# Kernel tuning notes

Measured on AMD Instinct MI355X. Metric: run time of the kernel, lower is better.

## Reference

```python
import jax, jax.numpy as jnp
import numpy as np

N_NODES = 50000
N_EDGES = 800000
IN_FT = 256
OUT_FT = 128


def setup_inputs() -> dict:
    key = jax.random.key(0)
    k_seq, k_src, k_dst, k_val, k_w = jax.random.split(key, 5)
    seq = jax.random.normal(k_seq, (N_NODES, IN_FT), dtype=jnp.float32)
    edge_src = jax.random.randint(k_src, (N_EDGES,), 0, N_NODES, dtype=jnp.int64)
    edge_dst = jax.random.randint(k_dst, (N_EDGES,), 0, N_NODES, dtype=jnp.int64)
    edge_val = jax.random.uniform(k_val, (N_EDGES,), dtype=jnp.float32)
    # xavier_uniform for Linear(in_ft, out_ft): limit = sqrt(6/(in+out))
    limit = float(np.sqrt(6.0 / (IN_FT + OUT_FT)))
    W = jax.random.uniform(k_w, (OUT_FT, IN_FT), minval=-limit, maxval=limit, dtype=jnp.float32)
    bias = jnp.zeros((OUT_FT,), dtype=jnp.float32)
    prelu_a = jnp.full((1,), 0.25, dtype=jnp.float32)  # nn.PReLU default slope
    return {"seq": seq, "edge_src": edge_src, "edge_dst": edge_dst,
            "edge_val": edge_val, "W": W, "bias": bias, "prelu_a": prelu_a}


def reference(seq, edge_src, edge_dst, edge_val, W, bias, prelu_a):
    # seq_fts = fc(seq): [N, out_ft]
    seq_fts = jnp.einsum('ni,oi->no', seq, W)
    # sparse spmm: out[dst] += val * seq_fts[src]
    msgs = seq_fts[edge_src] * edge_val[:, None]          # [E, out_ft]
    out = jax.ops.segment_sum(msgs, edge_dst, num_segments=seq.shape[0])
    out = out + bias                                       # bias add
    # PReLU with learnable slope a
    return jnp.where(out >= 0, out, prelu_a * out)
```

## Files before the change

### kernel.cpp

```cpp
#include <hip/hip_runtime.h>
#include <hip/hip_bf16.h>

#define N_NODES 50000
#define N_EDGES 800000
#define IN_FT 256
#define OUT_FT 128

typedef __bf16 bf16;
typedef __attribute__((ext_vector_type(8))) __bf16 bf16x8;
typedef __attribute__((ext_vector_type(4))) float floatx4;

static __device__ inline unsigned short f2bf_bits(float f) {
    unsigned u = __float_as_uint(f);
    return (unsigned short)((u + 0x7FFFu + ((u >> 16) & 1u)) >> 16);
}

#define P 256
#define CHUNK (N_EDGES / P)
#define NBUCK ((N_NODES + 255) / 256)
#define NSCAN (NBUCK * P)
#define GM 128
#define GEMM_BLKS ((N_NODES + GM - 1) / GM)
#define WP 264

__global__ __launch_bounds__(256) void k_prep(const float* __restrict__ W,
                                              const int* __restrict__ dst,
                                              unsigned short* __restrict__ Wb,
                                              int* __restrict__ cnt,
                                              unsigned long long* __restrict__ status,
                                              int* __restrict__ ticket) {
    const int b = blockIdx.x, t = threadIdx.x;
    if (b < P) {
        __shared__ int h[NBUCK];
        if (t < NBUCK) h[t] = 0;
        __syncthreads();
        const int base = b * CHUNK;
        for (int i = t; i < CHUNK; i += 256)
            atomicAdd(&h[dst[base + i] >> 8], 1);
        __syncthreads();
        if (t < NBUCK) cnt[t * P + b] = h[t];
    } else if (b == P) {
        if (t < NBUCK) status[t] = 0ull;
        if (t == 255) *ticket = 0;
    } else {
        int i = (b - P - 1) * 256 + t;
        float4 v = ((const float4*)W)[i];
        ushort4 o;
        o.x = f2bf_bits(v.x); o.y = f2bf_bits(v.y);
        o.z = f2bf_bits(v.z); o.w = f2bf_bits(v.w);
        ((ushort4*)Wb)[i] = o;
    }
}

__global__ __launch_bounds__(512) void k_gemm_scan(const float* __restrict__ seq,
                                                   const unsigned short* __restrict__ Wb,
                                                   unsigned short* __restrict__ seq_fts,
                                                   const int* __restrict__ cnt,
                                                   int* __restrict__ cnt_off,
                                                   int* __restrict__ partoff,
                                                   unsigned long long* __restrict__ status,
                                                   int* __restrict__ ticket) {
    const int t = threadIdx.x;
    if (blockIdx.x < GEMM_BLKS) {
        __shared__ bf16 Wlds[128 * WP];
        {
            const int row = t >> 2, c0 = (t & 3) * 64;
            const unsigned short* src = Wb + row * IN_FT + c0;
            bf16* dstp = Wlds + row * WP + c0;
#pragma unroll
            for (int c = 0; c < 8; ++c)
                *(uint4*)(dstp + c * 8) = *(const uint4*)(src + c * 8);
        }
        const int lane = t & 63;
        const int wave = t >> 6;
        const int quad = lane >> 4;
        const int l16  = lane & 15;

        int arow = blockIdx.x * GM + wave * 16 + l16;
        if (arow >= N_NODES) arow = 0;
        const float* ap = seq + (size_t)arow * IN_FT + quad * 8;
        bf16x8 afr[8];
#pragma unroll
        for (int s = 0; s < 8; ++s) {
            float4 v0 = *(const float4*)(ap + s * 32);
            float4 v1 = *(const float4*)(ap + s * 32 + 4);
            bf16x8 a;
            a[0] = (bf16)v0.x; a[1] = (bf16)v0.y; a[2] = (bf16)v0.z; a[3] = (bf16)v0.w;
            a[4] = (bf16)v1.x; a[5] = (bf16)v1.y; a[6] = (bf16)v1.z; a[7] = (bf16)v1.w;
            afr[s] = a;
        }
        __syncthreads();

        const int mbase = blockIdx.x * GM + wave * 16;
#pragma unroll
        for (int tt = 0; tt < 8; ++tt) {
            floatx4 acc = {0.f, 0.f, 0.f, 0.f};
            const bf16* bp = Wlds + (tt * 16 + l16) * WP + quad * 8;
#pragma unroll
            for (int s = 0; s < 8; ++s) {
                bf16x8 bfr = *(const bf16x8*)(bp + s * 32);
                acc = __builtin_amdgcn_mfma_f32_16x16x32_bf16(afr[s], bfr, acc, 0, 0, 0);
            }
#pragma unroll
            for (int r = 0; r < 4; ++r) {
                int m = mbase + quad * 4 + r;
                if (m < N_NODES)
                    seq_fts[(size_t)m * OUT_FT + tt * 16 + l16] = f2bf_bits(acc[r]);
            }
        }
    } else {
        __shared__ int lds2[256];
        __shared__ int stile;
        __shared__ unsigned run_sh;
        if (t == 0) stile = atomicAdd(ticket, 1);
        __syncthreads();
        const int j = stile;
        int v = (t < 256) ? cnt[j * 256 + t] : 0;
        if (t < 256) lds2[t] = v;
        __syncthreads();
        for (int s = 1; s < 256; s <<= 1) {
            int add = (t < 256 && t >= s) ? lds2[t - s] : 0;
            __syncthreads();
            if (t < 256) lds2[t] += add;
            __syncthreads();
        }
        const unsigned total = (unsigned)lds2[255];
        if (t == 0) {
            if (j == 0) {
                atomicExch(&status[0], ((unsigned long long)total << 2) | 2ull);
                run_sh = 0;
            } else {
                atomicExch(&status[j], ((unsigned long long)total << 2) | 1ull);
                unsigned running = 0;
                int k = j - 1;
                for (;;) {
                    unsigned long long s = atomicAdd(&status[k], 0ull);
                    unsigned st = (unsigned)(s & 3ull);
                    if (st == 0u) { __builtin_amdgcn_s_sleep(1); continue; }
                    running += (unsigned)(s >> 2);
                    if (st == 2u) break;
                    --k;
                }
                atomicExch(&status[j],
                           ((unsigned long long)(running + total) << 2) | 2ull);
                run_sh = running;
            }
        }
        __syncthreads();
        const int base = (int)run_sh;
        if (t < 256) cnt_off[j * 256 + t] = base + lds2[t] - v;
        if (t == 0) partoff[j] = base;
        if (t == 0 && j == NBUCK - 1) partoff[NBUCK] = base + (int)total;
    }
}

__global__ __launch_bounds__(256) void k_pscat(const int* __restrict__ src,
                                               const int* __restrict__ dst,
                                               const float* __restrict__ val,
                                               const int* __restrict__ cnt_off,
                                               uint2* __restrict__ part_ev) {
    __shared__ int off[NBUCK];
    const int t = threadIdx.x;
    if (t < NBUCK) off[t] = cnt_off[t * P + blockIdx.x];
    __syncthreads();
    const int base = blockIdx.x * CHUNK;
    for (int i = t; i < CHUNK; i += 256) {
        int e = base + i;
        int d = dst[e];
        int pos = atomicAdd(&off[d >> 8], 1);
        unsigned x = (unsigned)(unsigned short)src[e]
                   | ((unsigned)f2bf_bits(val[e]) << 16);
        part_ev[pos] = make_uint2(x, (unsigned)d);
    }
}

__global__ __launch_bounds__(256) void k_fill2(const uint2* __restrict__ part_ev,
                                               const int* __restrict__ partoff,
                                               int* __restrict__ row_ptr,
                                               unsigned* __restrict__ csr_ev) {
    __shared__ int cnt[256];
    __shared__ int lds[256];
    __shared__ int cur[256];
    const int b = blockIdx.x, t = threadIdx.x;
    const int start = partoff[b];
    const int end   = partoff[b + 1];
    cnt[t] = 0;
    __syncthreads();
    for (int i = start + t; i < end; i += 256)
        atomicAdd(&cnt[part_ev[i].y & 255u], 1);
    __syncthreads();
    int v = cnt[t];
    lds[t] = v;
    __syncthreads();
#pragma unroll
    for (int s = 1; s < 256; s <<= 1) {
        int t2 = (t >= s) ? lds[t - s] : 0;
        __syncthreads();
        lds[t] += t2;
        __syncthreads();
    }
    int base = start + lds[t] - v;
    int n = b * 256 + t;
    if (n <= N_NODES) row_ptr[n] = base;
    cur[t] = base;
    __syncthreads();
    for (int i = start + t; i < end; i += 256) {
        uint2 r = part_ev[i];
        int pos = atomicAdd(&cur[r.y & 255u], 1);
        csr_ev[pos] = r.x;
    }
}

#define GW 4
__global__ __launch_bounds__(64 * GW) void k_gather(const unsigned* __restrict__ fts,
                                                    const int* __restrict__ row_ptr,
                                                    const unsigned* __restrict__ csr_ev,
                                                    const float* __restrict__ bias,
                                                    const float* __restrict__ prelu_a,
                                                    float* __restrict__ out) {
    const int wave = threadIdx.x >> 6;
    const int lane = threadIdx.x & 63;
    const int n = blockIdx.x * GW + wave;
    if (n >= N_NODES) return;
    const int s0 = row_ptr[n];
    const int s1 = row_ptr[n + 1];
    float acc0 = 0.f, acc1 = 0.f;
    int j = s0;
    for (; j + 3 < s1; j += 4) {
        unsigned w0 = csr_ev[j],     w1 = csr_ev[j + 1];
        unsigned w2 = csr_ev[j + 2], w3 = csr_ev[j + 3];
        unsigned p0 = fts[(w0 & 0xFFFFu) * 64u + lane];
        unsigned p1 = fts[(w1 & 0xFFFFu) * 64u + lane];
        unsigned p2 = fts[(w2 & 0xFFFFu) * 64u + lane];
        unsigned p3 = fts[(w3 & 0xFFFFu) * 64u + lane];
        float v0 = __uint_as_float(w0 & 0xFFFF0000u);
        float v1 = __uint_as_float(w1 & 0xFFFF0000u);
        float v2 = __uint_as_float(w2 & 0xFFFF0000u);
        float v3 = __uint_as_float(w3 & 0xFFFF0000u);
        acc0 += v0 * __uint_as_float(p0 << 16);
        acc1 += v0 * __uint_as_float(p0 & 0xFFFF0000u);
        acc0 += v1 * __uint_as_float(p1 << 16);
        acc1 += v1 * __uint_as_float(p1 & 0xFFFF0000u);
        acc0 += v2 * __uint_as_float(p2 << 16);
        acc1 += v2 * __uint_as_float(p2 & 0xFFFF0000u);
        acc0 += v3 * __uint_as_float(p3 << 16);
        acc1 += v3 * __uint_as_float(p3 & 0xFFFF0000u);
    }
    for (; j < s1; ++j) {
        unsigned w0 = csr_ev[j];
        unsigned p0 = fts[(w0 & 0xFFFFu) * 64u + lane];
        float v0 = __uint_as_float(w0 & 0xFFFF0000u);
        acc0 += v0 * __uint_as_float(p0 << 16);
        acc1 += v0 * __uint_as_float(p0 & 0xFFFF0000u);
    }
    float2 b = *(const float2*)&bias[lane * 2];
    float a = prelu_a[0];
    float x0 = acc0 + b.x;
    float x1 = acc1 + b.y;
    x0 = (x0 >= 0.f) ? x0 : a * x0;
    x1 = (x1 >= 0.f) ? x1 : a * x1;
    *(float2*)&out[(size_t)n * OUT_FT + lane * 2] = make_float2(x0, x1);
}

extern "C" void kernel_launch(void* const* d_in, const int* in_sizes, int n_in,
                              void* d_out, int out_size, void* d_ws, size_t ws_size,
                              hipStream_t stream) {
    const float* seq      = (const float*)d_in[0];
    const int*   edge_src = (const int*)d_in[1];
    const int*   edge_dst = (const int*)d_in[2];
    const float* edge_val = (const float*)d_in[3];
    const float* W        = (const float*)d_in[4];
    const float* bias     = (const float*)d_in[5];
    const float* prelu_a  = (const float*)d_in[6];
    float* out = (float*)d_out;

    char* ws = (char*)d_ws;
    size_t off = 0;
    auto alloc = [&](size_t bytes) {
        void* p = ws + off;
        off = (off + bytes + 255) & ~(size_t)255;
        return p;
    };
    unsigned short* seq_fts = (unsigned short*)alloc((size_t)N_NODES * OUT_FT * sizeof(unsigned short));
    unsigned short* Wb      = (unsigned short*)alloc((size_t)OUT_FT * IN_FT * sizeof(unsigned short));
    int*   row_ptr = (int*)alloc((size_t)(N_NODES + 1) * sizeof(int));
    int*   cnt     = (int*)alloc((size_t)NSCAN * sizeof(int));
    int*   cnt_off = (int*)alloc((size_t)NSCAN * sizeof(int));
    int*   partoff = (int*)alloc((size_t)(NBUCK + 1) * sizeof(int));
    unsigned long long* status = (unsigned long long*)alloc((size_t)NBUCK * sizeof(unsigned long long));
    int*   ticket  = (int*)alloc(256);
    uint2* part_ev = (uint2*)alloc((size_t)N_EDGES * sizeof(uint2));
    unsigned* csr_ev = (unsigned*)alloc((size_t)N_EDGES * sizeof(unsigned));
    (void)ws_size; (void)in_sizes; (void)n_in; (void)out_size;

    k_prep<<<P + 1 + 32, 256, 0, stream>>>(W, edge_dst, Wb, cnt, status, ticket);
    k_gemm_scan<<<GEMM_BLKS + NBUCK, 512, 0, stream>>>(seq, Wb, seq_fts, cnt,
                                                       cnt_off, partoff, status, ticket);
    k_pscat<<<P, 256, 0, stream>>>(edge_src, edge_dst, edge_val, cnt_off, part_ev);
    k_fill2<<<NBUCK, 256, 0, stream>>>(part_ev, partoff, row_ptr, csr_ev);
    k_gather<<<(N_NODES + GW - 1) / GW, 64 * GW, 0, stream>>>((const unsigned*)seq_fts,
                                                              row_ptr, csr_ev,
                                                              bias, prelu_a, out);
}
```

Before: 181.0 us.

## Fuse CSR fill into gather and overlap partition scatter with GEMM

The bucket scan moves into its own small kernel, and the partition scatter now runs as extra blocks inside the GEMM launch so the two overlap. The CSR fill and the gather are merged into one kernel: each half-bucket block sorts its edges into LDS and accumulates rows directly. This removes the csr_ev/row_ptr global round trip and one launch. The cost is more passes over part_ev per bucket and an LDS capacity cap (GF_CAP) that silently drops edges if a half-bucket has more than 4096 of them. Each 512-thread block now handles only 128 nodes, which gives less gather parallelism.

```diff
diff --git a/kernel.cpp b/kernel.cpp
--- a/kernel.cpp
+++ b/kernel.cpp
@@ -22,6 +22,8 @@
 #define GM 128
 #define GEMM_BLKS ((N_NODES + GM - 1) / GM)
 #define WP 264
+#define PSB 128
+#define GF_CAP 4096
 
 __global__ __launch_bounds__(256) void k_prep(const float* __restrict__ W,
                                               const int* __restrict__ dst,
@@ -52,24 +54,74 @@
     }
 }
 
-__global__ __launch_bounds__(512) void k_gemm_scan(const float* __restrict__ seq,
-                                                   const unsigned short* __restrict__ Wb,
-                                                   unsigned short* __restrict__ seq_fts,
-                                                   const int* __restrict__ cnt,
-                                                   int* __restrict__ cnt_off,
-                                                   int* __restrict__ partoff,
-                                                   unsigned long long* __restrict__ status,
-                                                   int* __restrict__ ticket) {
+__global__ __launch_bounds__(256) void k_scan(const int* __restrict__ cnt,
+                                              int* __restrict__ cnt_off,
+                                              int* __restrict__ partoff,
+                                              unsigned long long* __restrict__ status,
+                                              int* __restrict__ ticket) {
+    __shared__ int lds2[256];
+    __shared__ int stile;
+    __shared__ unsigned run_sh;
+    const int t = threadIdx.x;
+    if (t == 0) stile = atomicAdd(ticket, 1);
+    __syncthreads();
+    const int j = stile;
+    int v = cnt[j * 256 + t];
+    lds2[t] = v;
+    __syncthreads();
+    for (int s = 1; s < 256; s <<= 1) {
+        int add = (t >= s) ? lds2[t - s] : 0;
+        __syncthreads();
+        lds2[t] += add;
+        __syncthreads();
+    }
+    const unsigned total = (unsigned)lds2[255];
+    if (t == 0) {
+        if (j == 0) {
+            atomicExch(&status[0], ((unsigned long long)total << 2) | 2ull);
+            run_sh = 0;
+        } else {
+            atomicExch(&status[j], ((unsigned long long)total << 2) | 1ull);
+            unsigned running = 0;
+            int k = j - 1;
+            for (;;) {
+                unsigned long long s = atomicAdd(&status[k], 0ull);
+                unsigned st = (unsigned)(s & 3ull);
+                if (st == 0u) { __builtin_amdgcn_s_sleep(1); continue; }
+                running += (unsigned)(s >> 2);
+                if (st == 2u) break;
+                --k;
+            }
+            atomicExch(&status[j],
+                       ((unsigned long long)(running + total) << 2) | 2ull);
+            run_sh = running;
+        }
+    }
+    __syncthreads();
+    const int base = (int)run_sh;
+    cnt_off[j * 256 + t] = base + lds2[t] - v;
+    if (t == 0) partoff[j] = base;
+    if (t == 0 && j == NBUCK - 1) partoff[NBUCK] = base + (int)total;
+}
+
+__global__ __launch_bounds__(512) void k_gemm_pscat(const float* __restrict__ seq,
+                                                    const unsigned short* __restrict__ Wb,
+                                                    unsigned short* __restrict__ seq_fts,
+                                                    const int* __restrict__ src,
+                                                    const int* __restrict__ dst,
+                                                    const float* __restrict__ val,
+                                                    const int* __restrict__ cnt_off,
+                                                    uint2* __restrict__ part_ev) {
     const int t = threadIdx.x;
     if (blockIdx.x < GEMM_BLKS) {
         __shared__ bf16 Wlds[128 * WP];
         {
             const int row = t >> 2, c0 = (t & 3) * 64;
-            const unsigned short* src = Wb + row * IN_FT + c0;
+            const unsigned short* srcp = Wb + row * IN_FT + c0;
             bf16* dstp = Wlds + row * WP + c0;
 #pragma unroll
             for (int c = 0; c < 8; ++c)
-                *(uint4*)(dstp + c * 8) = *(const uint4*)(src + c * 8);
+                *(uint4*)(dstp + c * 8) = *(const uint4*)(srcp + c * 8);
         }
         const int lane = t & 63;
         const int wave = t >> 6;
@@ -109,157 +161,116 @@
             }
         }
     } else {
-        __shared__ int lds2[256];
-        __shared__ int stile;
-        __shared__ unsigned run_sh;
-        if (t == 0) stile = atomicAdd(ticket, 1);
-        __syncthreads();
-        const int j = stile;
-        int v = (t < 256) ? cnt[j * 256 + t] : 0;
-        if (t < 256) lds2[t] = v;
-        __syncthreads();
-        for (int s = 1; s < 256; s <<= 1) {
-            int add = (t < 256 && t >= s) ? lds2[t - s] : 0;
-            __syncthreads();
-            if (t < 256) lds2[t] += add;
-            __syncthreads();
-        }
-        const unsigned total = (unsigned)lds2[255];
-        if (t == 0) {
-            if (j == 0) {
-                atomicExch(&status[0], ((unsigned long long)total << 2) | 2ull);
-                run_sh = 0;
-            } else {
-                atomicExch(&status[j], ((unsigned long long)total << 2) | 1ull);
-                unsigned running = 0;
-                int k = j - 1;
-                for (;;) {
-                    unsigned long long s = atomicAdd(&status[k], 0ull);
-                    unsigned st = (unsigned)(s & 3ull);
-                    if (st == 0u) { __builtin_amdgcn_s_sleep(1); continue; }
-                    running += (unsigned)(s >> 2);
-                    if (st == 2u) break;
-                    --k;
-                }
-                atomicExch(&status[j],
-                           ((unsigned long long)(running + total) << 2) | 2ull);
-                run_sh = running;
-            }
-        }
-        __syncthreads();
-        const int base = (int)run_sh;
-        if (t < 256) cnt_off[j * 256 + t] = base + lds2[t] - v;
-        if (t == 0) partoff[j] = base;
-        if (t == 0 && j == NBUCK - 1) partoff[NBUCK] = base + (int)total;
-    }
-}
-
-__global__ __launch_bounds__(256) void k_pscat(const int* __restrict__ src,
-                                               const int* __restrict__ dst,
-                                               const float* __restrict__ val,
-                                               const int* __restrict__ cnt_off,
-                                               uint2* __restrict__ part_ev) {
-    __shared__ int off[NBUCK];
-    const int t = threadIdx.x;
-    if (t < NBUCK) off[t] = cnt_off[t * P + blockIdx.x];
-    __syncthreads();
-    const int base = blockIdx.x * CHUNK;
-    for (int i = t; i < CHUNK; i += 256) {
-        int e = base + i;
-        int d = dst[e];
-        int pos = atomicAdd(&off[d >> 8], 1);
-        unsigned x = (unsigned)(unsigned short)src[e]
-                   | ((unsigned)f2bf_bits(val[e]) << 16);
-        part_ev[pos] = make_uint2(x, (unsigned)d);
-    }
-}
-
-__global__ __launch_bounds__(256) void k_fill2(const uint2* __restrict__ part_ev,
+        __shared__ int off2[2][NBUCK];
+        const int pb = blockIdx.x - GEMM_BLKS;
+        if (t < NBUCK)
+            off2[0][t] = cnt_off[t * P + 2 * pb];
+        else if (t >= 256 && t - 256 < NBUCK)
+            off2[1][t - 256] = cnt_off[(t - 256) * P + 2 * pb + 1];
+        __syncthreads();
+        const int c  = t >> 8;
+        const int tt = t & 255;
+        const int base = (2 * pb + c) * CHUNK;
+        for (int i = tt; i < CHUNK; i += 256) {
+            int e = base + i;
+            int d = dst[e];
+            int pos = atomicAdd(&off2[c][d >> 8], 1);
+            unsigned x = (unsigned)(unsigned short)src[e]
+                       | ((unsigned)f2bf_bits(val[e]) << 16);
+            part_ev[pos] = make_uint2(x, (unsigned)d);
+        }
+    }
+}
+
+__global__ __launch_bounds__(512) void k_gfill(const uint2* __restrict__ part_ev,
                                                const int* __restrict__ partoff,
-                                               int* __restrict__ row_ptr,
-                                               unsigned* __restrict__ csr_ev) {
-    __shared__ int cnt[256];
-    __shared__ int lds[256];
-    __shared__ int cur[256];
-    const int b = blockIdx.x, t = threadIdx.x;
+                                               const unsigned* __restrict__ fts,
+                                               const float* __restrict__ bias,
+                                               const float* __restrict__ prelu_a,
+                                               float* __restrict__ out) {
+    __shared__ unsigned pay[GF_CAP];
+    __shared__ int cnt[128], pfx[128], cur[128];
+    const int fb   = blockIdx.x;
+    const int b    = fb >> 1;
+    const int half = fb & 1;
+    const int t    = threadIdx.x;
     const int start = partoff[b];
     const int end   = partoff[b + 1];
-    cnt[t] = 0;
-    __syncthreads();
-    for (int i = start + t; i < end; i += 256)
-        atomicAdd(&cnt[part_ev[i].y & 255u], 1);
-    __syncthreads();
-    int v = cnt[t];
-    lds[t] = v;
-    __syncthreads();
-#pragma unroll
-    for (int s = 1; s < 256; s <<= 1) {
-        int t2 = (t >= s) ? lds[t - s] : 0;
-        __syncthreads();
-        lds[t] += t2;
-        __syncthreads();
-    }
-    int base = start + lds[t] - v;
-    int n = b * 256 + t;
-    if (n <= N_NODES) row_ptr[n] = base;
-    cur[t] = base;
-    __syncthreads();
-    for (int i = start + t; i < end; i += 256) {
+
+    if (t < 128) cnt[t] = 0;
+    __syncthreads();
+    for (int i = start + t; i < end; i += 512) {
+        unsigned rel = part_ev[i].y & 255u;
+        if ((int)(rel >> 7) == half) atomicAdd(&cnt[rel & 127u], 1);
+    }
+    __syncthreads();
+    if (t < 128) pfx[t] = cnt[t];
+    __syncthreads();
+#pragma unroll
+    for (int s = 1; s < 128; s <<= 1) {
+        int add = (t < 128 && t >= s) ? pfx[t - s] : 0;
+        __syncthreads();
+        if (t < 128) pfx[t] += add;
+        __syncthreads();
+    }
+    if (t < 128) cur[t] = pfx[t] - cnt[t];
+    __syncthreads();
+    for (int i = start + t; i < end; i += 512) {
         uint2 r = part_ev[i];
-        int pos = atomicAdd(&cur[r.y & 255u], 1);
-        csr_ev[pos] = r.x;
-    }
-}
-
-#define GW 4
-__global__ __launch_bounds__(64 * GW) void k_gather(const unsigned* __restrict__ fts,
-                                                    const int* __restrict__ row_ptr,
-                                                    const unsigned* __restrict__ csr_ev,
-                                                    const float* __restrict__ bias,
-                                                    const float* __restrict__ prelu_a,
-                                                    float* __restrict__ out) {
-    const int wave = threadIdx.x >> 6;
-    const int lane = threadIdx.x & 63;
-    const int n = blockIdx.x * GW + wave;
-    if (n >= N_NODES) return;
-    const int s0 = row_ptr[n];
-    const int s1 = row_ptr[n + 1];
-    float acc0 = 0.f, acc1 = 0.f;
-    int j = s0;
-    for (; j + 3 < s1; j += 4) {
-        unsigned w0 = csr_ev[j],     w1 = csr_ev[j + 1];
-        unsigned w2 = csr_ev[j + 2], w3 = csr_ev[j + 3];
-        unsigned p0 = fts[(w0 & 0xFFFFu) * 64u + lane];
-        unsigned p1 = fts[(w1 & 0xFFFFu) * 64u + lane];
-        unsigned p2 = fts[(w2 & 0xFFFFu) * 64u + lane];
-        unsigned p3 = fts[(w3 & 0xFFFFu) * 64u + lane];
-        float v0 = __uint_as_float(w0 & 0xFFFF0000u);
-        float v1 = __uint_as_float(w1 & 0xFFFF0000u);
-        float v2 = __uint_as_float(w2 & 0xFFFF0000u);
-        float v3 = __uint_as_float(w3 & 0xFFFF0000u);
-        acc0 += v0 * __uint_as_float(p0 << 16);
-        acc1 += v0 * __uint_as_float(p0 & 0xFFFF0000u);
-        acc0 += v1 * __uint_as_float(p1 << 16);
-        acc1 += v1 * __uint_as_float(p1 & 0xFFFF0000u);
-        acc0 += v2 * __uint_as_float(p2 << 16);
-        acc1 += v2 * __uint_as_float(p2 & 0xFFFF0000u);
-        acc0 += v3 * __uint_as_float(p3 << 16);
-        acc1 += v3 * __uint_as_float(p3 & 0xFFFF0000u);
-    }
-    for (; j < s1; ++j) {
-        unsigned w0 = csr_ev[j];
-        unsigned p0 = fts[(w0 & 0xFFFFu) * 64u + lane];
-        float v0 = __uint_as_float(w0 & 0xFFFF0000u);
-        acc0 += v0 * __uint_as_float(p0 << 16);
-        acc1 += v0 * __uint_as_float(p0 & 0xFFFF0000u);
-    }
-    float2 b = *(const float2*)&bias[lane * 2];
-    float a = prelu_a[0];
-    float x0 = acc0 + b.x;
-    float x1 = acc1 + b.y;
-    x0 = (x0 >= 0.f) ? x0 : a * x0;
-    x1 = (x1 >= 0.f) ? x1 : a * x1;
-    *(float2*)&out[(size_t)n * OUT_FT + lane * 2] = make_float2(x0, x1);
+        unsigned rel = r.y & 255u;
+        if ((int)(rel >> 7) == half) {
+            int pos = atomicAdd(&cur[rel & 127u], 1);
+            if (pos < GF_CAP) pay[pos] = r.x;
+        }
+    }
+    __syncthreads();
+
+    const int wave = t >> 6;
+    const int lane = t & 63;
+    const float2 bi = *(const float2*)&bias[lane * 2];
+    const float a = prelu_a[0];
+#pragma unroll
+    for (int q = 0; q < 16; ++q) {
+        const int ln = wave * 16 + q;
+        const int n  = b * 256 + half * 128 + ln;
+        if (n >= N_NODES) continue;
+        const int s1 = pfx[ln];
+        const int s0 = s1 - cnt[ln];
+        float acc0 = 0.f, acc1 = 0.f;
+        int j = s0;
+        for (; j + 3 < s1; j += 4) {
+            unsigned w0 = pay[j],     w1 = pay[j + 1];
+            unsigned w2 = pay[j + 2], w3 = pay[j + 3];
+            unsigned p0 = fts[(w0 & 0xFFFFu) * 64u + lane];
+            unsigned p1 = fts[(w1 & 0xFFFFu) * 64u + lane];
+            unsigned p2 = fts[(w2 & 0xFFFFu) * 64u + lane];
+            unsigned p3 = fts[(w3 & 0xFFFFu) * 64u + lane];
+            float v0 = __uint_as_float(w0 & 0xFFFF0000u);
+            float v1 = __uint_as_float(w1 & 0xFFFF0000u);
+            float v2 = __uint_as_float(w2 & 0xFFFF0000u);
+            float v3 = __uint_as_float(w3 & 0xFFFF0000u);
+            acc0 += v0 * __uint_as_float(p0 << 16);
+            acc1 += v0 * __uint_as_float(p0 & 0xFFFF0000u);
+            acc0 += v1 * __uint_as_float(p1 << 16);
+            acc1 += v1 * __uint_as_float(p1 & 0xFFFF0000u);
+            acc0 += v2 * __uint_as_float(p2 << 16);
+            acc1 += v2 * __uint_as_float(p2 & 0xFFFF0000u);
+            acc0 += v3 * __uint_as_float(p3 << 16);
+            acc1 += v3 * __uint_as_float(p3 & 0xFFFF0000u);
+        }
+        for (; j < s1; ++j) {
+            unsigned w0 = pay[j];
+            unsigned p0 = fts[(w0 & 0xFFFFu) * 64u + lane];
+            float v0 = __uint_as_float(w0 & 0xFFFF0000u);
+            acc0 += v0 * __uint_as_float(p0 << 16);
+            acc1 += v0 * __uint_as_float(p0 & 0xFFFF0000u);
+        }
+        float x0 = acc0 + bi.x;
+        float x1 = acc1 + bi.y;
+        x0 = (x0 >= 0.f) ? x0 : a * x0;
+        x1 = (x1 >= 0.f) ? x1 : a * x1;
+        *(float2*)&out[(size_t)n * OUT_FT + lane * 2] = make_float2(x0, x1);
+    }
 }
 
 extern "C" void kernel_launch(void* const* d_in, const int* in_sizes, int n_in,
@@ -283,22 +294,19 @@
     };
     unsigned short* seq_fts = (unsigned short*)alloc((size_t)N_NODES * OUT_FT * sizeof(unsigned short));
     unsigned short* Wb      = (unsigned short*)alloc((size_t)OUT_FT * IN_FT * sizeof(unsigned short));
-    int*   row_ptr = (int*)alloc((size_t)(N_NODES + 1) * sizeof(int));
     int*   cnt     = (int*)alloc((size_t)NSCAN * sizeof(int));
     int*   cnt_off = (int*)alloc((size_t)NSCAN * sizeof(int));
     int*   partoff = (int*)alloc((size_t)(NBUCK + 1) * sizeof(int));
     unsigned long long* status = (unsigned long long*)alloc((size_t)NBUCK * sizeof(unsigned long long));
     int*   ticket  = (int*)alloc(256);
     uint2* part_ev = (uint2*)alloc((size_t)N_EDGES * sizeof(uint2));
-    unsigned* csr_ev = (unsigned*)alloc((size_t)N_EDGES * sizeof(unsigned));
     (void)ws_size; (void)in_sizes; (void)n_in; (void)out_size;
 
     k_prep<<<P + 1 + 32, 256, 0, stream>>>(W, edge_dst, Wb, cnt, status, ticket);
-    k_gemm_scan<<<GEMM_BLKS + NBUCK, 512, 0, stream>>>(seq, Wb, seq_fts, cnt,
-                                                       cnt_off, partoff, status, ticket);
-    k_pscat<<<P, 256, 0, stream>>>(edge_src, edge_dst, edge_val, cnt_off, part_ev);
-    k_fill2<<<NBUCK, 256, 0, stream>>>(part_ev, partoff, row_ptr, csr_ev);
-    k_gather<<<(N_NODES + GW - 1) / GW, 64 * GW, 0, stream>>>((const unsigned*)seq_fts,
-                                                              row_ptr, csr_ev,
-                                                              bias, prelu_a, out);
-}
+    k_scan<<<NBUCK, 256, 0, stream>>>(cnt, cnt_off, partoff, status, ticket);
+    k_gemm_pscat<<<GEMM_BLKS + PSB, 512, 0, stream>>>(seq, Wb, seq_fts,
+                                                      edge_src, edge_dst, edge_val,
+                                                      cnt_off, part_ev);
+    k_gfill<<<NBUCK * 2, 512, 0, stream>>>(part_ev, partoff, (const unsigned*)seq_fts,
+                                           bias, prelu_a, out);
+}
```

Result: slower. 192.4 us (+6.3%).

## Move scan to own kernel and co-schedule partition scatter with GEMM

Applied to the files above, without the earlier changes.

Splits the decoupled-lookback bucket scan out into a standalone small kernel, and fuses the edge partition-scatter into the GEMM launch as extra blocks, each handling two chunks with 512 threads. The intent is to overlap the memory-bound scatter with the compute-bound GEMM rather than overlapping the tiny scan. The cost is an extra small kernel launch before the GEMM, and scatter blocks now share the GEMM's 512-thread, large-LDS block shape, which may limit occupancy.

```diff
diff --git a/kernel.cpp b/kernel.cpp
--- a/kernel.cpp
+++ b/kernel.cpp
@@ -22,6 +22,7 @@
 #define GM 128
 #define GEMM_BLKS ((N_NODES + GM - 1) / GM)
 #define WP 264
+#define PSB 128
 
 __global__ __launch_bounds__(256) void k_prep(const float* __restrict__ W,
                                               const int* __restrict__ dst,
@@ -52,24 +53,74 @@
     }
 }
 
-__global__ __launch_bounds__(512) void k_gemm_scan(const float* __restrict__ seq,
-                                                   const unsigned short* __restrict__ Wb,
-                                                   unsigned short* __restrict__ seq_fts,
-                                                   const int* __restrict__ cnt,
-                                                   int* __restrict__ cnt_off,
-                                                   int* __restrict__ partoff,
-                                                   unsigned long long* __restrict__ status,
-                                                   int* __restrict__ ticket) {
+__global__ __launch_bounds__(256) void k_scan(const int* __restrict__ cnt,
+                                              int* __restrict__ cnt_off,
+                                              int* __restrict__ partoff,
+                                              unsigned long long* __restrict__ status,
+                                              int* __restrict__ ticket) {
+    __shared__ int lds2[256];
+    __shared__ int stile;
+    __shared__ unsigned run_sh;
+    const int t = threadIdx.x;
+    if (t == 0) stile = atomicAdd(ticket, 1);
+    __syncthreads();
+    const int j = stile;
+    int v = cnt[j * 256 + t];
+    lds2[t] = v;
+    __syncthreads();
+    for (int s = 1; s < 256; s <<= 1) {
+        int add = (t >= s) ? lds2[t - s] : 0;
+        __syncthreads();
+        lds2[t] += add;
+        __syncthreads();
+    }
+    const unsigned total = (unsigned)lds2[255];
+    if (t == 0) {
+        if (j == 0) {
+            atomicExch(&status[0], ((unsigned long long)total << 2) | 2ull);
+            run_sh = 0;
+        } else {
+            atomicExch(&status[j], ((unsigned long long)total << 2) | 1ull);
+            unsigned running = 0;
+            int k = j - 1;
+            for (;;) {
+                unsigned long long s = atomicAdd(&status[k], 0ull);
+                unsigned st = (unsigned)(s & 3ull);
+                if (st == 0u) { __builtin_amdgcn_s_sleep(1); continue; }
+                running += (unsigned)(s >> 2);
+                if (st == 2u) break;
+                --k;
+            }
+            atomicExch(&status[j],
+                       ((unsigned long long)(running + total) << 2) | 2ull);
+            run_sh = running;
+        }
+    }
+    __syncthreads();
+    const int base = (int)run_sh;
+    cnt_off[j * 256 + t] = base + lds2[t] - v;
+    if (t == 0) partoff[j] = base;
+    if (t == 0 && j == NBUCK - 1) partoff[NBUCK] = base + (int)total;
+}
+
+__global__ __launch_bounds__(512) void k_gemm_pscat(const float* __restrict__ seq,
+                                                    const unsigned short* __restrict__ Wb,
+                                                    unsigned short* __restrict__ seq_fts,
+                                                    const int* __restrict__ src,
+                                                    const int* __restrict__ dst,
+                                                    const float* __restrict__ val,
+                                                    const int* __restrict__ cnt_off,
+                                                    uint2* __restrict__ part_ev) {
     const int t = threadIdx.x;
     if (blockIdx.x < GEMM_BLKS) {
         __shared__ bf16 Wlds[128 * WP];
         {
             const int row = t >> 2, c0 = (t & 3) * 64;
-            const unsigned short* src = Wb + row * IN_FT + c0;
+            const unsigned short* srcp = Wb + row * IN_FT + c0;
             bf16* dstp = Wlds + row * WP + c0;
 #pragma unroll
             for (int c = 0; c < 8; ++c)
-                *(uint4*)(dstp + c * 8) = *(const uint4*)(src + c * 8);
+                *(uint4*)(dstp + c * 8) = *(const uint4*)(srcp + c * 8);
         }
         const int lane = t & 63;
         const int wave = t >> 6;
@@ -109,68 +160,24 @@
             }
         }
     } else {
-        __shared__ int lds2[256];
-        __shared__ int stile;
-        __shared__ unsigned run_sh;
-        if (t == 0) stile = atomicAdd(ticket, 1);
-        __syncthreads();
-        const int j = stile;
-        int v = (t < 256) ? cnt[j * 256 + t] : 0;
-        if (t < 256) lds2[t] = v;
-        __syncthreads();
-        for (int s = 1; s < 256; s <<= 1) {
-            int add = (t < 256 && t >= s) ? lds2[t - s] : 0;
-            __syncthreads();
-            if (t < 256) lds2[t] += add;
-            __syncthreads();
-        }
-        const unsigned total = (unsigned)lds2[255];
-        if (t == 0) {
-            if (j == 0) {
-                atomicExch(&status[0], ((unsigned long long)total << 2) | 2ull);
-                run_sh = 0;
-            } else {
-                atomicExch(&status[j], ((unsigned long long)total << 2) | 1ull);
-                unsigned running = 0;
-                int k = j - 1;
-                for (;;) {
-                    unsigned long long s = atomicAdd(&status[k], 0ull);
-                    unsigned st = (unsigned)(s & 3ull);
-                    if (st == 0u) { __builtin_amdgcn_s_sleep(1); continue; }
-                    running += (unsigned)(s >> 2);
-                    if (st == 2u) break;
-                    --k;
-                }
-                atomicExch(&status[j],
-                           ((unsigned long long)(running + total) << 2) | 2ull);
-                run_sh = running;
-            }
-        }
-        __syncthreads();
-        const int base = (int)run_sh;
-        if (t < 256) cnt_off[j * 256 + t] = base + lds2[t] - v;
-        if (t == 0) partoff[j] = base;
-        if (t == 0 && j == NBUCK - 1) partoff[NBUCK] = base + (int)total;
-    }
-}
-
-__global__ __launch_bounds__(256) void k_pscat(const int* __restrict__ src,
-                                               const int* __restrict__ dst,
-                                               const float* __restrict__ val,
-                                               const int* __restrict__ cnt_off,
-                                               uint2* __restrict__ part_ev) {
-    __shared__ int off[NBUCK];
-    const int t = threadIdx.x;
-    if (t < NBUCK) off[t] = cnt_off[t * P + blockIdx.x];
-    __syncthreads();
-    const int base = blockIdx.x * CHUNK;
-    for (int i = t; i < CHUNK; i += 256) {
-        int e = base + i;
-        int d = dst[e];
-        int pos = atomicAdd(&off[d >> 8], 1);
-        unsigned x = (unsigned)(unsigned short)src[e]
-                   | ((unsigned)f2bf_bits(val[e]) << 16);
-        part_ev[pos] = make_uint2(x, (unsigned)d);
+        __shared__ int off2[2][NBUCK];
+        const int pb = blockIdx.x - GEMM_BLKS;
+        if (t < NBUCK)
+            off2[0][t] = cnt_off[t * P + 2 * pb];
+        else if (t >= 256 && t - 256 < NBUCK)
+            off2[1][t - 256] = cnt_off[(t - 256) * P + 2 * pb + 1];
+        __syncthreads();
+        const int c  = t >> 8;
+        const int tt = t & 255;
+        const int base = (2 * pb + c) * CHUNK;
+        for (int i = tt; i < CHUNK; i += 256) {
+            int e = base + i;
+            int d = dst[e];
+            int pos = atomicAdd(&off2[c][d >> 8], 1);
+            unsigned x = (unsigned)(unsigned short)src[e]
+                       | ((unsigned)f2bf_bits(val[e]) << 16);
+            part_ev[pos] = make_uint2(x, (unsigned)d);
+        }
     }
 }
 
@@ -294,9 +301,10 @@
     (void)ws_size; (void)in_sizes; (void)n_in; (void)out_size;
 
     k_prep<<<P + 1 + 32, 256, 0, stream>>>(W, edge_dst, Wb, cnt, status, ticket);
-    k_gemm_scan<<<GEMM_BLKS + NBUCK, 512, 0, stream>>>(seq, Wb, seq_fts, cnt,
-                                                       cnt_off, partoff, status, ticket);
-    k_pscat<<<P, 256, 0, stream>>>(edge_src, edge_dst, edge_val, cnt_off, part_ev);
+    k_scan<<<NBUCK, 256, 0, stream>>>(cnt, cnt_off, partoff, status, ticket);
+    k_gemm_pscat<<<GEMM_BLKS + PSB, 512, 0, stream>>>(seq, Wb, seq_fts,
+                                                      edge_src, edge_dst, edge_val,
+                                                      cnt_off, part_ev);
     k_fill2<<<NBUCK, 256, 0, stream>>>(part_ev, partoff, row_ptr, csr_ev);
     k_gather<<<(N_NODES + GW - 1) / GW, 64 * GW, 0, stream>>>((const unsigned*)seq_fts,
                                                               row_ptr, csr_ev,
```

New measurement: 186.6 us. 1.03x slower.
